# Kernel optimization log

Measured on AMD Instinct MI355X. Metric: run time of the kernel, lower is better.

The kernel has to match this reference:

```python
import jax, jax.numpy as jnp
import numpy as np

B, N, M = 1024, 65536, 128


def setup_inputs() -> dict:
    key = jax.random.key(0)
    k1, k2, k3, k4 = jax.random.split(key, 4)
    address = jax.random.uniform(k1, (B, N), dtype=jnp.float32)
    erase = jax.random.uniform(k2, (B, M), dtype=jnp.float32)
    add = jax.random.normal(k3, (B, M), dtype=jnp.float32)
    content = jax.random.uniform(k4, (N, M), dtype=jnp.float32)
    return {"address": address, "erase": erase, "add": add, "content": content}


def reference(address, erase, add, content):
    # write: outer-product erase/add aggregated over batch -> [N, M]
    erase_v = jnp.einsum('bn,bm->nm', address, erase)
    add_v = jnp.einsum('bn,bm->nm', address, add)
    new_content = content * (1.0 - erase_v) + add_v
    # read-after-write: [B,N] @ [N,M] -> [B,M]
    read_content = jnp.einsum('bn,nm->bm', address, new_content)
    return read_content
```

## Files before the change

### kernel.cpp

```cpp
#include <hip/hip_runtime.h>
#include <hip/hip_bf16.h>
#include <stdint.h>

#define B_SZ 1024
#define N_SZ 65536
#define M_SZ 128

typedef short bf16x8 __attribute__((ext_vector_type(8)));
typedef short bf16x4 __attribute__((ext_vector_type(4)));
typedef float f32x4 __attribute__((ext_vector_type(4)));

__device__ __forceinline__ unsigned short f2bf(float f) {
    uint32_t u = __float_as_uint(f);
    uint32_t r = (u + 0x7FFFu + ((u >> 16) & 1u)) >> 16;
    return (unsigned short)r;
}

__global__ __launch_bounds__(256) void k_edt(const float* __restrict__ E,
                                             const float* __restrict__ D,
                                             unsigned short* __restrict__ EDt) {
    __shared__ float tile[32][33];
    int bx = blockIdx.x & 31;
    int cy = blockIdx.x >> 5;
    int b0 = bx * 32, c0 = cy * 32;
    const float* src = (c0 < M_SZ) ? E : D;
    int cs0 = c0 & (M_SZ - 1);
    int t = threadIdx.x;
    int i = t >> 3, j = (t & 7) * 4;
    const float* p = src + (size_t)(b0 + i) * M_SZ + cs0 + j;
    float4 v = *(const float4*)p;
    tile[i][j] = v.x; tile[i][j + 1] = v.y; tile[i][j + 2] = v.z; tile[i][j + 3] = v.w;
    __syncthreads();
    int c = t >> 3, b4 = (t & 7) * 4;
    unsigned short* q = EDt + (size_t)(c0 + c) * B_SZ + b0 + b4;
    ushort4 o;
    o.x = f2bf(tile[b4 + 0][c]); o.y = f2bf(tile[b4 + 1][c]);
    o.z = f2bf(tile[b4 + 2][c]); o.w = f2bf(tile[b4 + 3][c]);
    *(ushort4*)q = o;
}

#define AS_LD 132
#define ED_LD 40

__global__ __launch_bounds__(256, 2) void k_pass1(
    const float* __restrict__ A,
    const unsigned short* __restrict__ EDt,
    const float* __restrict__ C,
    unsigned short* __restrict__ NCt)
{
    __shared__ __align__(16) unsigned short As[2][32 * AS_LD];
    __shared__ __align__(16) unsigned short EDs[2][256 * ED_LD];
    const int t = threadIdx.x;
    const int lane = t & 63;
    const int wv = t >> 6;
    const int wvn = wv >> 1, wvc = wv & 1;
    const int g = lane >> 4;
    const int m16 = lane & 15;
    const int n0 = blockIdx.x * 128;

    const int kb = t >> 3;
    const int cA = (t & 7) * 16;
    const int colq = t >> 3;
    const int seg = t & 7;

    int cb[8];
#pragma unroll
    for (int fj = 0; fj < 4; ++fj) { cb[fj] = wvc * 4 + fj; cb[fj + 4] = 8 + wvc * 4 + fj; }

    f32x4 acc[4][8];
#pragma unroll
    for (int i = 0; i < 4; ++i)
#pragma unroll
        for (int j = 0; j < 8; ++j) acc[i][j] = (f32x4){0.f, 0.f, 0.f, 0.f};

    {
        const float* p = A + (size_t)kb * N_SZ + n0 + cA;
        float4 a0 = ((const float4*)p)[0], a1 = ((const float4*)p)[1];
        float4 a2 = ((const float4*)p)[2], a3 = ((const float4*)p)[3];
        ushort4* w = (ushort4*)&As[0][kb * AS_LD + cA];
        ushort4 o;
        o.x = f2bf(a0.x); o.y = f2bf(a0.y); o.z = f2bf(a0.z); o.w = f2bf(a0.w); w[0] = o;
        o.x = f2bf(a1.x); o.y = f2bf(a1.y); o.z = f2bf(a1.z); o.w = f2bf(a1.w); w[1] = o;
        o.x = f2bf(a2.x); o.y = f2bf(a2.y); o.z = f2bf(a2.z); o.w = f2bf(a2.w); w[2] = o;
        o.x = f2bf(a3.x); o.y = f2bf(a3.y); o.z = f2bf(a3.z); o.w = f2bf(a3.w); w[3] = o;
#pragma unroll
        for (int p8 = 0; p8 < 8; ++p8) {
            int col = p8 * 32 + colq;
            ushort4 v = *(const ushort4*)(EDt + (size_t)col * B_SZ + seg * 4);
            *(ushort4*)&EDs[0][col * ED_LD + seg * 4] = v;
        }
    }
    __syncthreads();

    int cur = 0;
    for (int bk = 0; bk < B_SZ; bk += 32) {
        const bool last = (bk + 32 >= B_SZ);
        const int nk = last ? 0 : bk + 32;

        const float* p = A + (size_t)(nk + kb) * N_SZ + n0 + cA;
        float4 a0 = ((const float4*)p)[0], a1 = ((const float4*)p)[1];
        float4 a2 = ((const float4*)p)[2], a3 = ((const float4*)p)[3];
        ushort4 e[8];
#pragma unroll
        for (int p8 = 0; p8 < 8; ++p8) {
            int col = p8 * 32 + colq;
            e[p8] = *(const ushort4*)(EDt + (size_t)col * B_SZ + nk + seg * 4);
        }

        bf16x8 af[4];
#pragma unroll
        for (int fi = 0; fi < 4; ++fi) {
            int nl = wvn * 64 + fi * 16 + m16;
#pragma unroll
            for (int j = 0; j < 8; ++j)
                af[fi][j] = (short)As[cur][(g * 8 + j) * AS_LD + nl];
        }
        bf16x8 bfr[8];
#pragma unroll
        for (int fj = 0; fj < 8; ++fj)
            bfr[fj] = *(const bf16x8*)&EDs[cur][(cb[fj] * 16 + m16) * ED_LD + g * 8];

#pragma unroll
        for (int fj = 0; fj < 8; ++fj)
#pragma unroll
            for (int fi = 0; fi < 4; ++fi)
                acc[fi][fj] = __builtin_amdgcn_mfma_f32_16x16x32_bf16(af[fi], bfr[fj], acc[fi][fj], 0, 0, 0);

        if (!last) {
            const int nxt = cur ^ 1;
            ushort4* w = (ushort4*)&As[nxt][kb * AS_LD + cA];
            ushort4 o;
            o.x = f2bf(a0.x); o.y = f2bf(a0.y); o.z = f2bf(a0.z); o.w = f2bf(a0.w); w[0] = o;
            o.x = f2bf(a1.x); o.y = f2bf(a1.y); o.z = f2bf(a1.z); o.w = f2bf(a1.w); w[1] = o;
            o.x = f2bf(a2.x); o.y = f2bf(a2.y); o.z = f2bf(a2.z); o.w = f2bf(a2.w); w[2] = o;
            o.x = f2bf(a3.x); o.y = f2bf(a3.y); o.z = f2bf(a3.z); o.w = f2bf(a3.w); w[3] = o;
#pragma unroll
            for (int p8 = 0; p8 < 8; ++p8) {
                int col = p8 * 32 + colq;
                *(ushort4*)&EDs[nxt][col * ED_LD + seg * 4] = e[p8];
            }
        }
        __syncthreads();
        cur ^= 1;
    }

#pragma unroll
    for (int fi = 0; fi < 4; ++fi)
#pragma unroll
        for (int fj = 0; fj < 4; ++fj) {
            int n_base = n0 + wvn * 64 + fi * 16 + g * 4;
            int m = wvc * 64 + fj * 16 + m16;
            bf16x4 o;
#pragma unroll
            for (int r = 0; r < 4; ++r) {
                float w = acc[fi][fj][r];
                float v = acc[fi][fj + 4][r];
                float cc = C[(size_t)(n_base + r) * M_SZ + m];
                o[r] = (short)f2bf(cc * (1.0f - w) + v);
            }
            *(bf16x4*)&NCt[(size_t)m * N_SZ + n_base] = o;
        }
}

#define L2_LD 40

__global__ __launch_bounds__(256, 2) void k_pass2(
    const float* __restrict__ A,
    const unsigned short* __restrict__ NCt,
    float* __restrict__ part)
{
    __shared__ __align__(16) unsigned short As2[2][128 * L2_LD];
    __shared__ __align__(16) unsigned short NCs[2][128 * L2_LD];
    const int t = threadIdx.x;
    const int lane = t & 63;
    const int wv = t >> 6;
    const int wvb = wv >> 1, wvm = wv & 1;
    const int g = lane >> 4;
    const int m16 = lane & 15;
    const int b0 = (blockIdx.x & 7) * 128;
    const int ks = blockIdx.x >> 3;
    const int k0 = ks << 10;

    const int row = t >> 1, half = t & 1;

    f32x4 acc[4][4];
#pragma unroll
    for (int i = 0; i < 4; ++i)
#pragma unroll
        for (int j = 0; j < 4; ++j) acc[i][j] = (f32x4){0.f, 0.f, 0.f, 0.f};

    {
        const float* p = A + (size_t)(b0 + row) * N_SZ + k0 + half * 16;
        float4 a0 = ((const float4*)p)[0], a1 = ((const float4*)p)[1];
        float4 a2 = ((const float4*)p)[2], a3 = ((const float4*)p)[3];
        ushort4* w = (ushort4*)&As2[0][row * L2_LD + half * 16];
        ushort4 o;
        o.x = f2bf(a0.x); o.y = f2bf(a0.y); o.z = f2bf(a0.z); o.w = f2bf(a0.w); w[0] = o;
        o.x = f2bf(a1.x); o.y = f2bf(a1.y); o.z = f2bf(a1.z); o.w = f2bf(a1.w); w[1] = o;
        o.x = f2bf(a2.x); o.y = f2bf(a2.y); o.z = f2bf(a2.z); o.w = f2bf(a2.w); w[2] = o;
        o.x = f2bf(a3.x); o.y = f2bf(a3.y); o.z = f2bf(a3.z); o.w = f2bf(a3.w); w[3] = o;
        const uint4* pn = (const uint4*)(NCt + (size_t)row * N_SZ + k0 + half * 16);
        uint4 n0v = pn[0], n1v = pn[1];
        uint4* wn = (uint4*)&NCs[0][row * L2_LD + half * 16];
        wn[0] = n0v; wn[1] = n1v;
    }
    __syncthreads();

    int cur = 0;
    for (int kk = 0; kk < 1024; kk += 32) {
        const bool last = (kk + 32 >= 1024);
        const int nkk = last ? 0 : kk + 32;

        const float* p = A + (size_t)(b0 + row) * N_SZ + k0 + nkk + half * 16;
        float4 a0 = ((const float4*)p)[0], a1 = ((const float4*)p)[1];
        float4 a2 = ((const float4*)p)[2], a3 = ((const float4*)p)[3];
        const uint4* pn = (const uint4*)(NCt + (size_t)row * N_SZ + k0 + nkk + half * 16);
        uint4 n0v = pn[0], n1v = pn[1];

        bf16x8 af[4];
#pragma unroll
        for (int fi = 0; fi < 4; ++fi)
            af[fi] = *(const bf16x8*)&As2[cur][(wvb * 64 + fi * 16 + m16) * L2_LD + g * 8];
        bf16x8 bfr[4];
#pragma unroll
        for (int fj = 0; fj < 4; ++fj)
            bfr[fj] = *(const bf16x8*)&NCs[cur][(wvm * 64 + fj * 16 + m16) * L2_LD + g * 8];

#pragma unroll
        for (int fi = 0; fi < 4; ++fi)
#pragma unroll
            for (int fj = 0; fj < 4; ++fj)
                acc[fi][fj] = __builtin_amdgcn_mfma_f32_16x16x32_bf16(af[fi], bfr[fj], acc[fi][fj], 0, 0, 0);

        if (!last) {
            const int nxt = cur ^ 1;
            ushort4* w = (ushort4*)&As2[nxt][row * L2_LD + half * 16];
            ushort4 o;
            o.x = f2bf(a0.x); o.y = f2bf(a0.y); o.z = f2bf(a0.z); o.w = f2bf(a0.w); w[0] = o;
            o.x = f2bf(a1.x); o.y = f2bf(a1.y); o.z = f2bf(a1.z); o.w = f2bf(a1.w); w[1] = o;
            o.x = f2bf(a2.x); o.y = f2bf(a2.y); o.z = f2bf(a2.z); o.w = f2bf(a2.w); w[2] = o;
            o.x = f2bf(a3.x); o.y = f2bf(a3.y); o.z = f2bf(a3.z); o.w = f2bf(a3.w); w[3] = o;
            uint4* wn = (uint4*)&NCs[nxt][row * L2_LD + half * 16];
            wn[0] = n0v; wn[1] = n1v;
        }
        __syncthreads();
        cur ^= 1;
    }

    float* pp = part + (size_t)ks * (B_SZ * M_SZ);
#pragma unroll
    for (int fi = 0; fi < 4; ++fi)
#pragma unroll
        for (int fj = 0; fj < 4; ++fj)
#pragma unroll
            for (int r = 0; r < 4; ++r) {
                int b = b0 + wvb * 64 + fi * 16 + g * 4 + r;
                int m = wvm * 64 + fj * 16 + m16;
                pp[(size_t)b * M_SZ + m] = acc[fi][fj][r];
            }
}

__global__ __launch_bounds__(256) void k_reduce(const float* __restrict__ part,
                                                float* __restrict__ out) {
    const int idx4 = blockIdx.x * 256 + threadIdx.x;
    const float* p = part + (size_t)idx4 * 4;
    f32x4 s0 = {0.f,0.f,0.f,0.f}, s1 = s0, s2 = s0, s3 = s0;
#pragma unroll
    for (int s = 0; s < 64; s += 4) {
        f32x4 v0 = *(const f32x4*)(p + (size_t)(s + 0) * (B_SZ * M_SZ));
        f32x4 v1 = *(const f32x4*)(p + (size_t)(s + 1) * (B_SZ * M_SZ));
        f32x4 v2 = *(const f32x4*)(p + (size_t)(s + 2) * (B_SZ * M_SZ));
        f32x4 v3 = *(const f32x4*)(p + (size_t)(s + 3) * (B_SZ * M_SZ));
        s0 += v0; s1 += v1; s2 += v2; s3 += v3;
    }
    f32x4 r = (s0 + s1) + (s2 + s3);
    *(f32x4*)(out + (size_t)idx4 * 4) = r;
}

extern "C" void kernel_launch(void* const* d_in, const int* in_sizes, int n_in,
                              void* d_out, int out_size, void* d_ws, size_t ws_size,
                              hipStream_t stream) {
    const float* A  = (const float*)d_in[0];
    const float* E  = (const float*)d_in[1];
    const float* Dd = (const float*)d_in[2];
    const float* C  = (const float*)d_in[3];
    float* out = (float*)d_out;

    unsigned short* NCt = (unsigned short*)d_ws;
    unsigned short* EDt = (unsigned short*)((char*)d_ws + (size_t)M_SZ * N_SZ * 2);
    float* part = (float*)((char*)d_ws + (size_t)M_SZ * N_SZ * 2 + (size_t)256 * B_SZ * 2);

    k_edt   <<<256, 256, 0, stream>>>(E, Dd, EDt);
    k_pass1 <<<512, 256, 0, stream>>>(A, EDt, C, NCt);
    k_pass2 <<<512, 256, 0, stream>>>(A, NCt, part);
    k_reduce<<<128, 256, 0, stream>>>(part, out);
}
```

Before: 166.9 us.

## Load ED tile directly to LDS with swizzle and deepen A prefetch

The ED operand tile in pass1 is now copied straight from global memory into LDS with global_load_lds (16-byte) instead of being staged through registers. The LDS layout drops its padding and uses an XOR swizzle to avoid bank conflicts. The main loop is unrolled by two with explicit double-buffered register prefetch of A two steps ahead, so loads overlap the MFMA work. This cuts VGPR use and VALU copy instructions, at the cost of more complex indexing and a dependence on the direct-to-LDS path and the swizzle being correct.

```diff
diff --git a/kernel.cpp b/kernel.cpp
--- a/kernel.cpp
+++ b/kernel.cpp
@@ -40,7 +40,6 @@
 }
 
 #define AS_LD 132
-#define ED_LD 40
 
 __global__ __launch_bounds__(256, 2) void k_pass1(
     const float* __restrict__ A,
@@ -49,7 +48,7 @@
     unsigned short* __restrict__ NCt)
 {
     __shared__ __align__(16) unsigned short As[2][32 * AS_LD];
-    __shared__ __align__(16) unsigned short EDs[2][256 * ED_LD];
+    __shared__ __align__(16) unsigned short EDs[2][256 * 32];
     const int t = threadIdx.x;
     const int lane = t & 63;
     const int wv = t >> 6;
@@ -60,8 +59,6 @@
 
     const int kb = t >> 3;
     const int cA = (t & 7) * 16;
-    const int colq = t >> 3;
-    const int seg = t & 7;
 
     int cb[8];
 #pragma unroll
@@ -73,75 +70,83 @@
 #pragma unroll
         for (int j = 0; j < 8; ++j) acc[i][j] = (f32x4){0.f, 0.f, 0.f, 0.f};
 
-    {
-        const float* p = A + (size_t)kb * N_SZ + n0 + cA;
-        float4 a0 = ((const float4*)p)[0], a1 = ((const float4*)p)[1];
-        float4 a2 = ((const float4*)p)[2], a3 = ((const float4*)p)[3];
-        ushort4* w = (ushort4*)&As[0][kb * AS_LD + cA];
-        ushort4 o;
-        o.x = f2bf(a0.x); o.y = f2bf(a0.y); o.z = f2bf(a0.z); o.w = f2bf(a0.w); w[0] = o;
-        o.x = f2bf(a1.x); o.y = f2bf(a1.y); o.z = f2bf(a1.z); o.w = f2bf(a1.w); w[1] = o;
-        o.x = f2bf(a2.x); o.y = f2bf(a2.y); o.z = f2bf(a2.z); o.w = f2bf(a2.w); w[2] = o;
-        o.x = f2bf(a3.x); o.y = f2bf(a3.y); o.z = f2bf(a3.z); o.w = f2bf(a3.w); w[3] = o;
-#pragma unroll
-        for (int p8 = 0; p8 < 8; ++p8) {
-            int col = p8 * 32 + colq;
-            ushort4 v = *(const ushort4*)(EDt + (size_t)col * B_SZ + seg * 4);
-            *(ushort4*)&EDs[0][col * ED_LD + seg * 4] = v;
+#define ED_GLLDS(buf, bkv)                                                          \
+    {                                                                               \
+        _Pragma("unroll")                                                           \
+        for (int i_ = 0; i_ < 4; ++i_) {                                            \
+            int L_ = i_ * 256 + t;                                                  \
+            int col_ = L_ >> 2;                                                     \
+            int ss_ = (L_ & 3) ^ ((col_ >> 1) & 3);                                 \
+            const unsigned short* gsrc_ = EDt + (size_t)col_ * B_SZ + (bkv) + ss_ * 8; \
+            __builtin_amdgcn_global_load_lds(                                       \
+                (const __attribute__((address_space(1))) uint32_t*)(const void*)gsrc_, \
+                (__attribute__((address_space(3))) uint32_t*)(void*)&EDs[buf][(i_ * 256 + wv * 64) * 8], \
+                16, 0, 0);                                                          \
+        }                                                                           \
+    }
+
+#define A_LOAD(dst0, dst1, dst2, dst3, bkv)                                         \
+    {                                                                               \
+        const float* p_ = A + (size_t)((bkv) + kb) * N_SZ + n0 + cA;                \
+        dst0 = ((const float4*)p_)[0]; dst1 = ((const float4*)p_)[1];               \
+        dst2 = ((const float4*)p_)[2]; dst3 = ((const float4*)p_)[3];               \
+    }
+
+#define A_WRITE(buf, s0, s1, s2, s3)                                                \
+    {                                                                               \
+        ushort4* w_ = (ushort4*)&As[buf][kb * AS_LD + cA];                          \
+        ushort4 o_;                                                                 \
+        o_.x = f2bf(s0.x); o_.y = f2bf(s0.y); o_.z = f2bf(s0.z); o_.w = f2bf(s0.w); w_[0] = o_; \
+        o_.x = f2bf(s1.x); o_.y = f2bf(s1.y); o_.z = f2bf(s1.z); o_.w = f2bf(s1.w); w_[1] = o_; \
+        o_.x = f2bf(s2.x); o_.y = f2bf(s2.y); o_.z = f2bf(s2.z); o_.w = f2bf(s2.w); w_[2] = o_; \
+        o_.x = f2bf(s3.x); o_.y = f2bf(s3.y); o_.z = f2bf(s3.z); o_.w = f2bf(s3.w); w_[3] = o_; \
+    }
+
+#define P1_COMPUTE(buf)                                                             \
+    {                                                                               \
+        bf16x8 af_[4];                                                              \
+        _Pragma("unroll")                                                           \
+        for (int fi = 0; fi < 4; ++fi) {                                            \
+            int nl_ = wvn * 64 + fi * 16 + m16;                                     \
+            _Pragma("unroll")                                                       \
+            for (int j = 0; j < 8; ++j)                                             \
+                af_[fi][j] = (short)As[buf][(g * 8 + j) * AS_LD + nl_];              \
+        }                                                                           \
+        bf16x8 bfr_[8];                                                             \
+        _Pragma("unroll")                                                           \
+        for (int fj = 0; fj < 8; ++fj) {                                            \
+            int col_ = cb[fj] * 16 + m16;                                           \
+            bfr_[fj] = *(const bf16x8*)&EDs[buf][col_ * 32 + ((g ^ ((col_ >> 1) & 3)) << 3)]; \
+        }                                                                           \
+        _Pragma("unroll")                                                           \
+        for (int fj = 0; fj < 8; ++fj)                                              \
+            _Pragma("unroll")                                                       \
+            for (int fi = 0; fi < 4; ++fi)                                          \
+                acc[fi][fj] = __builtin_amdgcn_mfma_f32_16x16x32_bf16(af_[fi], bfr_[fj], acc[fi][fj], 0, 0, 0); \
+    }
+
+    float4 ra0_0, ra0_1, ra0_2, ra0_3;
+    float4 ra1_0, ra1_1, ra1_2, ra1_3;
+
+    A_LOAD(ra0_0, ra0_1, ra0_2, ra0_3, 0)
+    ED_GLLDS(0, 0)
+    A_WRITE(0, ra0_0, ra0_1, ra0_2, ra0_3)
+    A_LOAD(ra1_0, ra1_1, ra1_2, ra1_3, 32)
+    __syncthreads();
+
+    for (int c = 0; c < 32; c += 2) {
+        if (c + 1 < 32) ED_GLLDS(1, (c + 1) * 32)
+        if (c + 2 < 32) A_LOAD(ra0_0, ra0_1, ra0_2, ra0_3, (c + 2) * 32)
+        P1_COMPUTE(0)
+        if (c + 1 < 32) A_WRITE(1, ra1_0, ra1_1, ra1_2, ra1_3)
+        __syncthreads();
+        if (c + 1 < 32) {
+            if (c + 2 < 32) ED_GLLDS(0, (c + 2) * 32)
+            if (c + 3 < 32) A_LOAD(ra1_0, ra1_1, ra1_2, ra1_3, (c + 3) * 32)
+            P1_COMPUTE(1)
+            if (c + 2 < 32) A_WRITE(0, ra0_0, ra0_1, ra0_2, ra0_3)
+            __syncthreads();
         }
-    }
-    __syncthreads();
-
-    int cur = 0;
-    for (int bk = 0; bk < B_SZ; bk += 32) {
-        const bool last = (bk + 32 >= B_SZ);
-        const int nk = last ? 0 : bk + 32;
-
-        const float* p = A + (size_t)(nk + kb) * N_SZ + n0 + cA;
-        float4 a0 = ((const float4*)p)[0], a1 = ((const float4*)p)[1];
-        float4 a2 = ((const float4*)p)[2], a3 = ((const float4*)p)[3];
-        ushort4 e[8];
-#pragma unroll
-        for (int p8 = 0; p8 < 8; ++p8) {
-            int col = p8 * 32 + colq;
-            e[p8] = *(const ushort4*)(EDt + (size_t)col * B_SZ + nk + seg * 4);
-        }
-
-        bf16x8 af[4];
-#pragma unroll
-        for (int fi = 0; fi < 4; ++fi) {
-            int nl = wvn * 64 + fi * 16 + m16;
-#pragma unroll
-            for (int j = 0; j < 8; ++j)
-                af[fi][j] = (short)As[cur][(g * 8 + j) * AS_LD + nl];
-        }
-        bf16x8 bfr[8];
-#pragma unroll
-        for (int fj = 0; fj < 8; ++fj)
-            bfr[fj] = *(const bf16x8*)&EDs[cur][(cb[fj] * 16 + m16) * ED_LD + g * 8];
-
-#pragma unroll
-        for (int fj = 0; fj < 8; ++fj)
-#pragma unroll
-            for (int fi = 0; fi < 4; ++fi)
-                acc[fi][fj] = __builtin_amdgcn_mfma_f32_16x16x32_bf16(af[fi], bfr[fj], acc[fi][fj], 0, 0, 0);
-
-        if (!last) {
-            const int nxt = cur ^ 1;
-            ushort4* w = (ushort4*)&As[nxt][kb * AS_LD + cA];
-            ushort4 o;
-            o.x = f2bf(a0.x); o.y = f2bf(a0.y); o.z = f2bf(a0.z); o.w = f2bf(a0.w); w[0] = o;
-            o.x = f2bf(a1.x); o.y = f2bf(a1.y); o.z = f2bf(a1.z); o.w = f2bf(a1.w); w[1] = o;
-            o.x = f2bf(a2.x); o.y = f2bf(a2.y); o.z = f2bf(a2.z); o.w = f2bf(a2.w); w[2] = o;
-            o.x = f2bf(a3.x); o.y = f2bf(a3.y); o.z = f2bf(a3.z); o.w = f2bf(a3.w); w[3] = o;
-#pragma unroll
-            for (int p8 = 0; p8 < 8; ++p8) {
-                int col = p8 * 32 + colq;
-                *(ushort4*)&EDs[nxt][col * ED_LD + seg * 4] = e[p8];
-            }
-        }
-        __syncthreads();
-        cur ^= 1;
     }
 
 #pragma unroll
```

Result: faster. 152.0 us (-8.9%).
